# Kernel tuning notes

Measured on AMD Instinct MI355X. Metric: run time of the kernel, lower is better.

The kernel has to match this reference:

```python
import jax, jax.numpy as jnp
import numpy as np
from jax import lax

T, N, E = 12, 10000, 160000
C_IN, C_H, C_OUT = 32, 64, 32
EPS = 1e-5


def _glorot(key, shape):
    fan_in, fan_out = shape[-2] if len(shape) > 1 else shape[0], shape[-1]
    s = (6.0 / (fan_in + fan_out)) ** 0.5
    return jax.random.uniform(key, shape, jnp.float32, -s, s)


def setup_inputs() -> dict:
    key = jax.random.key(0)
    ks = jax.random.split(key, 16)
    inp = {
        "x": jax.random.normal(ks[0], (T, N, C_IN), jnp.float32),
        "edge_index": jax.random.randint(ks[1], (2, E), 0, N, jnp.int32),
        "edge_weight": jax.random.uniform(ks[2], (E,), jnp.float32),
        # layer 1 (input layer): in=C_IN -> C_H
        "conv_w1": _glorot(ks[3], (C_H, C_IN, 3)) * 0.1,
        "conv_b1": jnp.zeros((C_H,), jnp.float32),
        "gamma1": jnp.ones((C_H,), jnp.float32),
        "beta1": jnp.zeros((C_H,), jnp.float32),
        "gcn_w1": _glorot(ks[4], (C_H, C_H)),
        "gcn_b1": jnp.zeros((C_H,), jnp.float32),
        # layer 2 (hidden layer): C_H -> C_H
        "conv_w2": _glorot(ks[5], (C_H, C_H, 3)) * 0.1,
        "conv_b2": jnp.zeros((C_H,), jnp.float32),
        "gamma2": jnp.ones((C_H,), jnp.float32),
        "beta2": jnp.zeros((C_H,), jnp.float32),
        "gcn_w2": _glorot(ks[6], (C_H, C_H)),
        "gcn_b2": jnp.zeros((C_H,), jnp.float32),
        # output linear: C_H -> C_OUT
        "out_w": _glorot(ks[7], (C_H, C_OUT)),
        "out_b": jnp.zeros((C_OUT,), jnp.float32),
    }
    return inp


def _stgcn_layer(x, edge_index, edge_weight, cw, cb, gamma, beta, gw, gb):
    # x: [T, N, C_in]  ->  torch.stack(x).permute(1,2,0) = [N, C_in, T]
    xs = jnp.transpose(x, (1, 2, 0))
    h = lax.conv_general_dilated(xs, cw, (1,), [(1, 1)],
                                 dimension_numbers=("NCH", "OIH", "NCH"))
    h = h + cb[None, :, None]
    # InstanceNorm1d(affine) over the temporal dim
    mu = h.mean(-1, keepdims=True)
    var = ((h - mu) ** 2).mean(-1, keepdims=True)
    h = (h - mu) * lax.rsqrt(var + EPS) * gamma[None, :, None] + beta[None, :, None]
    h = jax.nn.relu(h)
    h = jnp.transpose(h, (2, 0, 1))  # [T, N, C_out]
    # GCNConv per timestep (vectorized over T)
    src, dst = edge_index[0], edge_index[1]
    n = h.shape[1]
    deg = jnp.zeros((n,), h.dtype).at[dst].add(edge_weight) + 1.0  # self-loop weight 1
    dis = lax.rsqrt(deg)
    norm = dis[src] * edge_weight * dis[dst]  # [E]
    xw = jnp.einsum("tnc,cd->tnd", h, gw)  # [T, N, C_out]
    msg = xw[:, src, :] * norm[None, :, None]  # [T, E, C_out]
    agg = jax.vmap(lambda m: jax.ops.segment_sum(m, dst, num_segments=n))(msg)
    agg = agg + (dis * dis)[None, :, None] * xw + gb  # self loop + bias
    return agg


def reference(x, edge_index, edge_weight,
              conv_w1, conv_b1, gamma1, beta1, gcn_w1, gcn_b1,
              conv_w2, conv_b2, gamma2, beta2, gcn_w2, gcn_b2,
              out_w, out_b):
    h = _stgcn_layer(x, edge_index, edge_weight,
                     conv_w1, conv_b1, gamma1, beta1, gcn_w1, gcn_b1)
    h = _stgcn_layer(h, edge_index, edge_weight,
                     conv_w2, conv_b2, gamma2, beta2, gcn_w2, gcn_b2)
    out = jnp.einsum("tnc,co->tno", h, out_w) + out_b  # per-t linear
    return out.mean(axis=0)  # [N, C_OUT]
```

## Files before the change

kernel.cpp:

```cpp
#include <hip/hip_runtime.h>
#include <hip/hip_bf16.h>
#include <stdint.h>

#define MAXDEG 64

typedef short s16x8 __attribute__((ext_vector_type(8)));
typedef short s16x4 __attribute__((ext_vector_type(4)));
typedef float f32x4 __attribute__((ext_vector_type(4)));

static __device__ __forceinline__ float us2f(unsigned short u) {
    union { float f; unsigned int i; } cv; cv.i = ((unsigned int)u) << 16; return cv.f;
}
static __device__ __forceinline__ unsigned short f2us(float f) {
    __hip_bfloat16 h = __float2bfloat16(f);
    return *(unsigned short*)&h;
}

#define WIMG_TOTAL 30720

__global__ void k_prep(const float* __restrict__ cw1, const float* __restrict__ gw1,
                       const float* __restrict__ cw2, const float* __restrict__ gw2,
                       unsigned short* __restrict__ wimg)
{
    int idx = blockIdx.x * 256 + threadIdx.x;
    if (idx >= WIMG_TOTAL) return;
    float v = 0.f;
    if (idx < 7680) {
        int kk = idx / 2560, r = idx - kk * 2560, cc = r / 40, ci = r - cc * 40;
        if (ci < 32) v = cw1[(cc * 32 + ci) * 3 + kk];
    } else if (idx < 12288) {
        int j = idx - 7680, d = j / 72, cc = j - d * 72;
        if (cc < 64) v = gw1[cc * 64 + d];
    } else if (idx < 26112) {
        int j = idx - 12288;
        int kk = j / 4608, r = j - kk * 4608, cc = r / 72, ci = r - cc * 72;
        if (ci < 64) v = cw2[(cc * 64 + ci) * 3 + kk];
    } else {
        int j = idx - 26112, d = j / 72, cc = j - d * 72;
        if (cc < 64) v = gw2[cc * 64 + d];
    }
    wimg[idx] = f2us(v);
}

#define BLO(u) __uint_as_float((unsigned)(u) << 16)
#define BHI(u) __uint_as_float((unsigned)(u) & 0xffff0000u)

#define ACC2(NRM, WA, WB)                                                              \
    a[0] = fmaf(NRM, BLO(WA.x), a[0]);   a[1] = fmaf(NRM, BHI(WA.x), a[1]);            \
    a[2] = fmaf(NRM, BLO(WA.y), a[2]);   a[3] = fmaf(NRM, BHI(WA.y), a[3]);            \
    a[4] = fmaf(NRM, BLO(WA.z), a[4]);   a[5] = fmaf(NRM, BHI(WA.z), a[5]);            \
    a[6] = fmaf(NRM, BLO(WA.w), a[6]);   a[7] = fmaf(NRM, BHI(WA.w), a[7]);            \
    a[8] = fmaf(NRM, us2f(WB.x), a[8]);  a[9] = fmaf(NRM, us2f(WB.y), a[9]);           \
    a[10] = fmaf(NRM, us2f(WB.z), a[10]); a[11] = fmaf(NRM, us2f(WB.w), a[11]);

template<int CIN>
__global__ __launch_bounds__(1024, 4) void k_layer_build(
    const float* __restrict__ x_in,
    const unsigned short* __restrict__ wimg,
    const float* __restrict__ gm, const float* __restrict__ bt,
    unsigned short* __restrict__ xw_out, int N, int NB,
    const int* __restrict__ ei, const float* __restrict__ ew,
    float* __restrict__ deg, unsigned* __restrict__ cnt,
    int2* __restrict__ ell, int E)
{
    if ((int)blockIdx.x >= NB) {
        int e = ((int)blockIdx.x - NB) * 1024 + (int)threadIdx.x;
        if (e < E) {
            int s = ei[e], d = ei[E + e];
            float w = ew[e];
            atomicAdd(&deg[d], w);
            unsigned slot = atomicAdd(&cnt[d], 1u);
            if (slot < MAXDEG) ell[(size_t)d * MAXDEG + slot] = make_int2(s, __float_as_int(w));
        }
        return;
    }

    constexpr int KT   = CIN / 32;
    constexpr int WSTR = (CIN == 64) ? 72 : 40;
    __shared__ __align__(16) short WT[3 * 64 * WSTR];
    __shared__ __align__(16) short gwT[64 * 72];
    __shared__ __align__(16) short xh[16][14 * 72];

    const int tid = threadIdx.x;
    const int nn = tid >> 6;
    const int c = tid & 63;
    const int m = c & 15;
    const int q = c >> 4;
    const int mrow = (m < 12) ? m : 11;
    int n = blockIdx.x * 16 + nn;
    if (n >= N) n = N - 1;

    {
        const uint4* wt1  = (const uint4*)(wimg);
        const uint4* gwt1 = (const uint4*)(wimg + 7680);
        if (tid < 960) ((uint4*)WT)[tid]  = wt1[tid];
        if (tid < 576) ((uint4*)gwT)[tid] = gwt1[tid];
    }
    #pragma unroll
    for (int it = 0; it < (12 * CIN) / 128; ++it) {
        int i2 = it * 128 + c * 2;
        int t = i2 / CIN, ci = i2 - t * CIN;
        float2 xv = *(const float2*)&x_in[((size_t)t * N + n) * CIN + ci];
        xh[nn][(t + 1) * 72 + ci]     = (short)f2us(xv.x);
        xh[nn][(t + 1) * 72 + ci + 1] = (short)f2us(xv.y);
    }
    if (c < CIN) { xh[nn][c] = 0; xh[nn][13 * 72 + c] = 0; }
    __syncthreads();

    f32x4 acc[4];
    #pragma unroll
    for (int nt = 0; nt < 4; ++nt) acc[nt] = (f32x4){0.f, 0.f, 0.f, 0.f};
    #pragma unroll
    for (int kk = 0; kk < 3; ++kk) {
        #pragma unroll
        for (int kt = 0; kt < KT; ++kt) {
            s16x8 aA = *(const s16x8*)&xh[nn][(mrow + kk) * 72 + kt * 32 + q * 8];
            #pragma unroll
            for (int nt = 0; nt < 4; ++nt) {
                s16x8 bB = *(const s16x8*)&WT[kk * (64 * WSTR) + (nt * 16 + m) * WSTR + kt * 32 + q * 8];
                acc[nt] = __builtin_amdgcn_mfma_f32_16x16x32_bf16(aA, bB, acc[nt], 0, 0, 0);
            }
        }
    }

    #pragma unroll
    for (int nt = 0; nt < 4; ++nt) {
        float s  = acc[nt][0] + acc[nt][1] + acc[nt][2] + acc[nt][3];
        float s2 = acc[nt][0] * acc[nt][0] + acc[nt][1] * acc[nt][1]
                 + acc[nt][2] * acc[nt][2] + acc[nt][3] * acc[nt][3];
        if (q == 3) { s = 0.f; s2 = 0.f; }
        s  += __shfl_xor(s, 16);  s  += __shfl_xor(s, 32);
        s2 += __shfl_xor(s2, 16); s2 += __shfl_xor(s2, 32);
        const float mu  = s * (1.f / 12.f);
        const float var = s2 * (1.f / 12.f) - mu * mu;
        const float scn = rsqrtf(var + 1e-5f) * gm[nt * 16 + m];
        const float sbn = bt[nt * 16 + m];
        if (q < 3) {
            #pragma unroll
            for (int reg = 0; reg < 4; ++reg) {
                float hv = fmaf(acc[nt][reg] - mu, scn, sbn);
                hv = hv > 0.f ? hv : 0.f;
                xh[nn][(q * 4 + reg) * 72 + nt * 16 + m] = (short)f2us(hv);
            }
        }
    }

    s16x8 a2[2];
    #pragma unroll
    for (int kt2 = 0; kt2 < 2; ++kt2)
        a2[kt2] = *(const s16x8*)&xh[nn][mrow * 72 + kt2 * 32 + q * 8];
    f32x4 acc2[4];
    #pragma unroll
    for (int nt = 0; nt < 4; ++nt) acc2[nt] = (f32x4){0.f, 0.f, 0.f, 0.f};
    #pragma unroll
    for (int nt = 0; nt < 4; ++nt) {
        #pragma unroll
        for (int kt2 = 0; kt2 < 2; ++kt2) {
            s16x8 b2 = *(const s16x8*)&gwT[(nt * 16 + m) * 72 + kt2 * 32 + q * 8];
            acc2[nt] = __builtin_amdgcn_mfma_f32_16x16x32_bf16(a2[kt2], b2, acc2[nt], 0, 0, 0);
        }
    }

    unsigned short* dst = xw_out + (size_t)n * 768;
    if (q < 3) {
        #pragma unroll
        for (int nt = 0; nt < 4; ++nt)
            #pragma unroll
            for (int reg = 0; reg < 4; ++reg)
                dst[(q * 4 + reg) * 64 + nt * 16 + m] = f2us(acc2[nt][reg]);
    }
}

__global__ __launch_bounds__(512, 4) void k_gather_a(
    const unsigned short* __restrict__ xw_in,
    const int2* __restrict__ ell, const unsigned* __restrict__ cnt,
    const float* __restrict__ deg, const float* __restrict__ gb,
    const unsigned short* __restrict__ wimg,
    const float* __restrict__ gm, const float* __restrict__ bt,
    unsigned short* __restrict__ rowmean, int N)
{
    constexpr int WSTR = 72;
    __shared__ __align__(16) short WT[3 * 64 * WSTR];
    __shared__ __align__(16) short gwT[64 * 72];
    __shared__ __align__(16) short xh[8][14 * 72];

    const int tid = threadIdx.x;
    const int nn = tid >> 6;
    const int L = tid & 63;
    const int m = L & 15;
    const int q = L >> 4;
    const int mrow = (m < 12) ? m : 11;
    int n = blockIdx.x * 8 + nn;
    if (n >= N) n = N - 1;

    const int2* row = ell + (size_t)n * MAXDEG;
    int2 pl = row[L];
    unsigned dg = cnt[n]; if (dg > MAXDEG) dg = MAXDEG;
    const float dn = rsqrtf(deg[n] + 1.0f);
    const float d2 = dn * dn;
    const unsigned short* sp = xw_in + (size_t)n * 768;
    uint4   sA = *(const uint4*)(sp + 8 * L);
    ushort4 sB = *(const ushort4*)(sp + 512 + 4 * L);

    {
        const uint4* wt2  = (const uint4*)(wimg + 12288);
        const uint4* gwt2 = (const uint4*)(wimg + 26112);
        for (int g = tid; g < 1728; g += 512) ((uint4*)WT)[g]  = wt2[g];
        for (int g = tid; g < 576;  g += 512) ((uint4*)gwT)[g] = gwt2[g];
    }
    xh[nn][L] = 0; xh[nn][13 * 72 + L] = 0;
    __syncthreads();

    float a[12];
    {
        const int cb1 = 8 * (L & 7);
        const int cb2 = (4 * L) & 63;
        a[0] = fmaf(d2, BLO(sA.x), gb[cb1 + 0]); a[1] = fmaf(d2, BHI(sA.x), gb[cb1 + 1]);
        a[2] = fmaf(d2, BLO(sA.y), gb[cb1 + 2]); a[3] = fmaf(d2, BHI(sA.y), gb[cb1 + 3]);
        a[4] = fmaf(d2, BLO(sA.z), gb[cb1 + 4]); a[5] = fmaf(d2, BHI(sA.z), gb[cb1 + 5]);
        a[6] = fmaf(d2, BLO(sA.w), gb[cb1 + 6]); a[7] = fmaf(d2, BHI(sA.w), gb[cb1 + 7]);
        a[8] = fmaf(d2, us2f(sB.x), gb[cb2 + 0]); a[9]  = fmaf(d2, us2f(sB.y), gb[cb2 + 1]);
        a[10] = fmaf(d2, us2f(sB.z), gb[cb2 + 2]); a[11] = fmaf(d2, us2f(sB.w), gb[cb2 + 3]);
    }

    unsigned e = 0;
    for (; e + 8 <= dg; e += 8) {
        uint4 A[8]; ushort4 Bv[8]; float NR[8];
        #pragma unroll
        for (int i = 0; i < 8; ++i) {
            unsigned sxr = (unsigned)__builtin_amdgcn_readlane(pl.x, (int)(e + i));
            float w = __int_as_float(__builtin_amdgcn_readlane(pl.y, (int)(e + i)));
            unsigned sx = (sxr < (unsigned)N) ? sxr : 0u;
            float nr = rsqrtf(deg[sx] + 1.0f) * w * dn;
            NR[i] = (sxr < (unsigned)N) ? nr : 0.f;
            const unsigned short* qp = xw_in + (size_t)sx * 768;
            A[i]  = *(const uint4*)(qp + 8 * L);
            Bv[i] = *(const ushort4*)(qp + 512 + 4 * L);
        }
        #pragma unroll
        for (int i = 0; i < 8; ++i) { ACC2(NR[i], A[i], Bv[i]) }
    }
    if (e + 4 <= dg) {
        uint4 A[4]; ushort4 Bv[4]; float NR[4];
        #pragma unroll
        for (int i = 0; i < 4; ++i) {
            unsigned sxr = (unsigned)__builtin_amdgcn_readlane(pl.x, (int)(e + i));
            float w = __int_as_float(__builtin_amdgcn_readlane(pl.y, (int)(e + i)));
            unsigned sx = (sxr < (unsigned)N) ? sxr : 0u;
            float nr = rsqrtf(deg[sx] + 1.0f) * w * dn;
            NR[i] = (sxr < (unsigned)N) ? nr : 0.f;
            const unsigned short* qp = xw_in + (size_t)sx * 768;
            A[i]  = *(const uint4*)(qp + 8 * L);
            Bv[i] = *(const ushort4*)(qp + 512 + 4 * L);
        }
        #pragma unroll
        for (int i = 0; i < 4; ++i) { ACC2(NR[i], A[i], Bv[i]) }
        e += 4;
    }
    for (; e < dg; ++e) {
        unsigned sxr = (unsigned)__builtin_amdgcn_readlane(pl.x, (int)e);
        float w = __int_as_float(__builtin_amdgcn_readlane(pl.y, (int)e));
        unsigned sx = (sxr < (unsigned)N) ? sxr : 0u;
        float nr = rsqrtf(deg[sx] + 1.0f) * w * dn;
        if (sxr >= (unsigned)N) nr = 0.f;
        const unsigned short* qp = xw_in + (size_t)sx * 768;
        uint4 A = *(const uint4*)(qp + 8 * L);
        ushort4 Bv = *(const ushort4*)(qp + 512 + 4 * L);
        ACC2(nr, A, Bv)
    }

    {
        s16x8 p1 = { (short)f2us(a[0]), (short)f2us(a[1]), (short)f2us(a[2]), (short)f2us(a[3]),
                     (short)f2us(a[4]), (short)f2us(a[5]), (short)f2us(a[6]), (short)f2us(a[7]) };
        *(s16x8*)&xh[nn][((L >> 3) + 1) * 72 + 8 * (L & 7)] = p1;
        s16x4 p2 = { (short)f2us(a[8]), (short)f2us(a[9]), (short)f2us(a[10]), (short)f2us(a[11]) };
        *(s16x4*)&xh[nn][((L >> 4) + 9) * 72 + ((4 * L) & 63)] = p2;
    }

    f32x4 acc[4];
    #pragma unroll
    for (int nt = 0; nt < 4; ++nt) acc[nt] = (f32x4){0.f, 0.f, 0.f, 0.f};
    #pragma unroll
    for (int kk = 0; kk < 3; ++kk) {
        #pragma unroll
        for (int kt = 0; kt < 2; ++kt) {
            s16x8 aA = *(const s16x8*)&xh[nn][(mrow + kk) * 72 + kt * 32 + q * 8];
            #pragma unroll
            for (int nt = 0; nt < 4; ++nt) {
                s16x8 bB = *(const s16x8*)&WT[kk * (64 * WSTR) + (nt * 16 + m) * WSTR + kt * 32 + q * 8];
                acc[nt] = __builtin_amdgcn_mfma_f32_16x16x32_bf16(aA, bB, acc[nt], 0, 0, 0);
            }
        }
    }

    #pragma unroll
    for (int nt = 0; nt < 4; ++nt) {
        float s  = acc[nt][0] + acc[nt][1] + acc[nt][2] + acc[nt][3];
        float s2 = acc[nt][0] * acc[nt][0] + acc[nt][1] * acc[nt][1]
                 + acc[nt][2] * acc[nt][2] + acc[nt][3] * acc[nt][3];
        if (q == 3) { s = 0.f; s2 = 0.f; }
        s  += __shfl_xor(s, 16);  s  += __shfl_xor(s, 32);
        s2 += __shfl_xor(s2, 16); s2 += __shfl_xor(s2, 32);
        const float mu  = s * (1.f / 12.f);
        const float var = s2 * (1.f / 12.f) - mu * mu;
        const float scn = rsqrtf(var + 1e-5f) * gm[nt * 16 + m];
        const float sbn = bt[nt * 16 + m];
        if (q < 3) {
            #pragma unroll
            for (int reg = 0; reg < 4; ++reg) {
                float hv = fmaf(acc[nt][reg] - mu, scn, sbn);
                hv = hv > 0.f ? hv : 0.f;
                xh[nn][(q * 4 + reg) * 72 + nt * 16 + m] = (short)f2us(hv);
            }
        }
    }

    s16x8 a2[2];
    #pragma unroll
    for (int kt2 = 0; kt2 < 2; ++kt2)
        a2[kt2] = *(const s16x8*)&xh[nn][mrow * 72 + kt2 * 32 + q * 8];
    f32x4 acc2[4];
    #pragma unroll
    for (int nt = 0; nt < 4; ++nt) acc2[nt] = (f32x4){0.f, 0.f, 0.f, 0.f};
    #pragma unroll
    for (int nt = 0; nt < 4; ++nt) {
        #pragma unroll
        for (int kt2 = 0; kt2 < 2; ++kt2) {
            s16x8 b2 = *(const s16x8*)&gwT[(nt * 16 + m) * 72 + kt2 * 32 + q * 8];
            acc2[nt] = __builtin_amdgcn_mfma_f32_16x16x32_bf16(a2[kt2], b2, acc2[nt], 0, 0, 0);
        }
    }

    #pragma unroll
    for (int nt = 0; nt < 4; ++nt) {
        float pm = (q < 3) ? (acc2[nt][0] + acc2[nt][1] + acc2[nt][2] + acc2[nt][3]) : 0.f;
        pm += __shfl_xor(pm, 16); pm += __shfl_xor(pm, 32);
        if (q == 0)
            rowmean[(size_t)n * 64 + nt * 16 + m] = f2us(pm * (1.f / 12.f));
    }
}

#define FIN_E(EIDX)                                                                    \
    {                                                                                  \
        unsigned sxr = (unsigned)__builtin_amdgcn_readlane(pl.x, (int)(EIDX));         \
        float w = __int_as_float(__builtin_amdgcn_readlane(pl.y, (int)(EIDX)));        \
        unsigned sx = (sxr < (unsigned)N) ? sxr : 0u;                                  \
        float nr = rsqrtf(deg[sx] + 1.0f) * w * dn;                                    \
        if (sxr >= (unsigned)N) nr = 0.f;                                              \
        a = fmaf(nr, us2f(rowmean[(size_t)sx * 64 + L]), a);                           \
    }

__global__ __launch_bounds__(256) void k_final(
    const unsigned short* __restrict__ rowmean, const int2* __restrict__ ell,
    const unsigned* __restrict__ cnt, const float* __restrict__ deg,
    const float* __restrict__ gb,
    const float* __restrict__ ow, const float* __restrict__ ob,
    float* __restrict__ dout, int N)
{
    __shared__ __align__(16) float hbuf[4][64];
    const int tid = threadIdx.x;
    const int nn = tid >> 6, L = tid & 63;
    int n = blockIdx.x * 4 + nn;
    if (n >= N) n = N - 1;
    const float dn = rsqrtf(deg[n] + 1.0f);
    const float d2 = dn * dn;

    const int2* row = ell + (size_t)n * MAXDEG;
    int2 pl = row[L];
    unsigned dg = cnt[n]; if (dg > MAXDEG) dg = MAXDEG;

    float a = fmaf(d2, us2f(rowmean[(size_t)n * 64 + L]), gb[L]);

    unsigned e = 0;
    for (; e + 7 < dg; e += 8) {
        FIN_E(e)     FIN_E(e + 1) FIN_E(e + 2) FIN_E(e + 3)
        FIN_E(e + 4) FIN_E(e + 5) FIN_E(e + 6) FIN_E(e + 7)
    }
    for (; e < dg; ++e) { FIN_E(e) }

    hbuf[nn][L] = a;
    __syncthreads();
    if (L < 32) {
        float oa = ob[L];
        #pragma unroll
        for (int cc = 0; cc < 64; ++cc)
            oa = fmaf(hbuf[nn][cc], ow[cc * 32 + L], oa);
        dout[(size_t)n * 32 + L] = oa;
    }
}

extern "C" void kernel_launch(void* const* d_in, const int* in_sizes, int n_in,
                              void* d_out, int out_size, void* d_ws, size_t ws_size,
                              hipStream_t stream)
{
    const float* x   = (const float*)d_in[0];
    const int*   ei  = (const int*)d_in[1];
    const float* ew  = (const float*)d_in[2];
    const float* cw1 = (const float*)d_in[3];
    const float* gm1 = (const float*)d_in[5];
    const float* bt1 = (const float*)d_in[6];
    const float* gw1 = (const float*)d_in[7];
    const float* gb1 = (const float*)d_in[8];
    const float* cw2 = (const float*)d_in[9];
    const float* gm2 = (const float*)d_in[11];
    const float* bt2 = (const float*)d_in[12];
    const float* gw2 = (const float*)d_in[13];
    const float* gb2 = (const float*)d_in[14];
    const float* ow  = (const float*)d_in[15];
    const float* ob  = (const float*)d_in[16];

    const int N = in_sizes[0] / (12 * 32);
    const int E = in_sizes[2];

    char* p0 = (char*)d_ws;
    char* p = p0;
    float* deg = (float*)p;          p += (size_t)N * 4;
    unsigned* cnt = (unsigned*)p;    p += (size_t)N * 4;
    p = (char*)(((uintptr_t)p + 255) & ~(uintptr_t)255);
    int2* ell = (int2*)p;            p += (size_t)N * MAXDEG * 8;
    p = (char*)(((uintptr_t)p + 255) & ~(uintptr_t)255);
    unsigned short* wimg = (unsigned short*)p; p += (size_t)WIMG_TOTAL * 2;
    p = (char*)(((uintptr_t)p + 255) & ~(uintptr_t)255);
    unsigned short* bufXW1 = (unsigned short*)p; p += (size_t)N * 768 * 2;
    unsigned short* rowmean = (unsigned short*)p; p += (size_t)N * 64 * 2;

    const size_t need = (size_t)(p - p0);
    if (ws_size < need) {
        hipMemsetAsync(d_out, 0, (size_t)out_size * 4, stream);
        return;
    }

    hipMemsetAsync(deg, 0, (size_t)N * 8, stream);

    const int nb16 = (N + 15) / 16;
    const int ebb  = (E + 1023) / 1024;
    const int nb8  = (N + 7) / 8;
    const int nb4  = (N + 3) / 4;
    k_prep<<<(WIMG_TOTAL + 255) / 256, 256, 0, stream>>>(cw1, gw1, cw2, gw2, wimg);

    k_layer_build<32><<<nb16 + ebb, 1024, 0, stream>>>(x, wimg, gm1, bt1, bufXW1, N, nb16,
                                                       ei, ew, deg, cnt, ell, E);
    k_gather_a<<<nb8, 512, 0, stream>>>(bufXW1, ell, cnt, deg, gb1,
                                        wimg, gm2, bt2, rowmean, N);
    k_final<<<nb4, 256, 0, stream>>>(rowmean, ell, cnt, deg, gb2, ow, ob, (float*)d_out, N);
}
```

Before: 169.6 us.

## Fold output linear into layer-2 GCN weight and aggregate 32-wide rowmeans

Precomputes gw2·out_w (64x32) and a constant bias gb2·out_w+ob in the prep kernel, so layer 2 produces 32-channel projected rowmeans instead of 64. The final gather then reads half as much data per neighbor and drops the per-node 64x32 matvec and its shared-memory sync. The deg/cnt zeroing memset is also folded into the prep kernel to remove one launch. The fused weight is rounded to bf16, which changes rounding slightly.

```diff
diff --git a/kernel.cpp b/kernel.cpp
--- a/kernel.cpp
+++ b/kernel.cpp
@@ -16,30 +16,47 @@
     return *(unsigned short*)&h;
 }
 
-#define WIMG_TOTAL 30720
+#define WIMG_TOTAL 28416
 
 __global__ void k_prep(const float* __restrict__ cw1, const float* __restrict__ gw1,
                        const float* __restrict__ cw2, const float* __restrict__ gw2,
-                       unsigned short* __restrict__ wimg)
+                       const float* __restrict__ gb2, const float* __restrict__ ow,
+                       const float* __restrict__ ob,
+                       unsigned short* __restrict__ wimg, float* __restrict__ c0f,
+                       unsigned* __restrict__ zbase, int zwords)
 {
     int idx = blockIdx.x * 256 + threadIdx.x;
-    if (idx >= WIMG_TOTAL) return;
-    float v = 0.f;
-    if (idx < 7680) {
-        int kk = idx / 2560, r = idx - kk * 2560, cc = r / 40, ci = r - cc * 40;
-        if (ci < 32) v = cw1[(cc * 32 + ci) * 3 + kk];
-    } else if (idx < 12288) {
-        int j = idx - 7680, d = j / 72, cc = j - d * 72;
-        if (cc < 64) v = gw1[cc * 64 + d];
-    } else if (idx < 26112) {
-        int j = idx - 12288;
-        int kk = j / 4608, r = j - kk * 4608, cc = r / 72, ci = r - cc * 72;
-        if (ci < 64) v = cw2[(cc * 64 + ci) * 3 + kk];
-    } else {
-        int j = idx - 26112, d = j / 72, cc = j - d * 72;
-        if (cc < 64) v = gw2[cc * 64 + d];
-    }
-    wimg[idx] = f2us(v);
+    if (idx < WIMG_TOTAL) {
+        float v = 0.f;
+        if (idx < 7680) {
+            int kk = idx / 2560, r = idx - kk * 2560, cc = r / 40, ci = r - cc * 40;
+            if (ci < 32) v = cw1[(cc * 32 + ci) * 3 + kk];
+        } else if (idx < 12288) {
+            int j = idx - 7680, d = j / 72, cc = j - d * 72;
+            if (cc < 64) v = gw1[cc * 64 + d];
+        } else if (idx < 26112) {
+            int j = idx - 12288;
+            int kk = j / 4608, r = j - kk * 4608, cc = r / 72, ci = r - cc * 72;
+            if (ci < 64) v = cw2[(cc * 64 + ci) * 3 + kk];
+        } else {
+            int j = idx - 26112, o = j / 72, cc = j - o * 72;
+            if (cc < 64) {
+                float s = 0.f;
+                #pragma unroll 8
+                for (int d = 0; d < 64; ++d) s = fmaf(gw2[cc * 64 + d], ow[d * 32 + o], s);
+                v = s;
+            }
+        }
+        wimg[idx] = f2us(v);
+    } else if (idx < WIMG_TOTAL + 32) {
+        int o = idx - WIMG_TOTAL;
+        float s = ob[o];
+        #pragma unroll 8
+        for (int c = 0; c < 64; ++c) s = fmaf(gb2[c], ow[c * 32 + o], s);
+        c0f[o] = s;
+    } else if (idx - (WIMG_TOTAL + 32) < zwords) {
+        zbase[idx - (WIMG_TOTAL + 32)] = 0u;
+    }
 }
 
 #define BLO(u) __uint_as_float((unsigned)(u) << 16)
@@ -177,11 +194,11 @@
     const float* __restrict__ deg, const float* __restrict__ gb,
     const unsigned short* __restrict__ wimg,
     const float* __restrict__ gm, const float* __restrict__ bt,
-    unsigned short* __restrict__ rowmean, int N)
+    unsigned short* __restrict__ rm32, int N)
 {
     constexpr int WSTR = 72;
     __shared__ __align__(16) short WT[3 * 64 * WSTR];
-    __shared__ __align__(16) short gwT[64 * 72];
+    __shared__ __align__(16) short gwT[32 * 72];
     __shared__ __align__(16) short xh[8][14 * 72];
 
     const int tid = threadIdx.x;
@@ -204,9 +221,9 @@
 
     {
         const uint4* wt2  = (const uint4*)(wimg + 12288);
-        const uint4* gwt2 = (const uint4*)(wimg + 26112);
+        const uint4* gwp  = (const uint4*)(wimg + 26112);
         for (int g = tid; g < 1728; g += 512) ((uint4*)WT)[g]  = wt2[g];
-        for (int g = tid; g < 576;  g += 512) ((uint4*)gwT)[g] = gwt2[g];
+        if (tid < 288) ((uint4*)gwT)[tid] = gwp[tid];
     }
     xh[nn][L] = 0; xh[nn][13 * 72 + L] = 0;
     __syncthreads();
@@ -319,11 +336,11 @@
     #pragma unroll
     for (int kt2 = 0; kt2 < 2; ++kt2)
         a2[kt2] = *(const s16x8*)&xh[nn][mrow * 72 + kt2 * 32 + q * 8];
-    f32x4 acc2[4];
-    #pragma unroll
-    for (int nt = 0; nt < 4; ++nt) acc2[nt] = (f32x4){0.f, 0.f, 0.f, 0.f};
-    #pragma unroll
-    for (int nt = 0; nt < 4; ++nt) {
+    f32x4 acc2[2];
+    acc2[0] = (f32x4){0.f, 0.f, 0.f, 0.f};
+    acc2[1] = (f32x4){0.f, 0.f, 0.f, 0.f};
+    #pragma unroll
+    for (int nt = 0; nt < 2; ++nt) {
         #pragma unroll
         for (int kt2 = 0; kt2 < 2; ++kt2) {
             s16x8 b2 = *(const s16x8*)&gwT[(nt * 16 + m) * 72 + kt2 * 32 + q * 8];
@@ -332,11 +349,11 @@
     }
 
     #pragma unroll
-    for (int nt = 0; nt < 4; ++nt) {
+    for (int nt = 0; nt < 2; ++nt) {
         float pm = (q < 3) ? (acc2[nt][0] + acc2[nt][1] + acc2[nt][2] + acc2[nt][3]) : 0.f;
         pm += __shfl_xor(pm, 16); pm += __shfl_xor(pm, 32);
         if (q == 0)
-            rowmean[(size_t)n * 64 + nt * 16 + m] = f2us(pm * (1.f / 12.f));
+            rm32[(size_t)n * 32 + nt * 16 + m] = f2us(pm * (1.f / 12.f));
     }
 }
 
@@ -347,19 +364,18 @@
         unsigned sx = (sxr < (unsigned)N) ? sxr : 0u;                                  \
         float nr = rsqrtf(deg[sx] + 1.0f) * w * dn;                                    \
         if (sxr >= (unsigned)N) nr = 0.f;                                              \
-        a = fmaf(nr, us2f(rowmean[(size_t)sx * 64 + L]), a);                           \
+        a = fmaf(nr, us2f(rm32[(size_t)sx * 32 + o]), a);                              \
     }
 
 __global__ __launch_bounds__(256) void k_final(
-    const unsigned short* __restrict__ rowmean, const int2* __restrict__ ell,
+    const unsigned short* __restrict__ rm32, const int2* __restrict__ ell,
     const unsigned* __restrict__ cnt, const float* __restrict__ deg,
-    const float* __restrict__ gb,
-    const float* __restrict__ ow, const float* __restrict__ ob,
+    const float* __restrict__ c0f,
     float* __restrict__ dout, int N)
 {
-    __shared__ __align__(16) float hbuf[4][64];
     const int tid = threadIdx.x;
     const int nn = tid >> 6, L = tid & 63;
+    const int o = L & 31;
     int n = blockIdx.x * 4 + nn;
     if (n >= N) n = N - 1;
     const float dn = rsqrtf(deg[n] + 1.0f);
@@ -369,7 +385,7 @@
     int2 pl = row[L];
     unsigned dg = cnt[n]; if (dg > MAXDEG) dg = MAXDEG;
 
-    float a = fmaf(d2, us2f(rowmean[(size_t)n * 64 + L]), gb[L]);
+    float a = fmaf(d2, us2f(rm32[(size_t)n * 32 + o]), c0f[o]);
 
     unsigned e = 0;
     for (; e + 7 < dg; e += 8) {
@@ -378,15 +394,7 @@
     }
     for (; e < dg; ++e) { FIN_E(e) }
 
-    hbuf[nn][L] = a;
-    __syncthreads();
-    if (L < 32) {
-        float oa = ob[L];
-        #pragma unroll
-        for (int cc = 0; cc < 64; ++cc)
-            oa = fmaf(hbuf[nn][cc], ow[cc * 32 + L], oa);
-        dout[(size_t)n * 32 + L] = oa;
-    }
+    if (L < 32) dout[(size_t)n * 32 + o] = a;
 }
 
 extern "C" void kernel_launch(void* const* d_in, const int* in_sizes, int n_in,
@@ -421,8 +429,10 @@
     p = (char*)(((uintptr_t)p + 255) & ~(uintptr_t)255);
     unsigned short* wimg = (unsigned short*)p; p += (size_t)WIMG_TOTAL * 2;
     p = (char*)(((uintptr_t)p + 255) & ~(uintptr_t)255);
+    float* c0f = (float*)p;          p += 32 * 4;
+    p = (char*)(((uintptr_t)p + 255) & ~(uintptr_t)255);
     unsigned short* bufXW1 = (unsigned short*)p; p += (size_t)N * 768 * 2;
-    unsigned short* rowmean = (unsigned short*)p; p += (size_t)N * 64 * 2;
+    unsigned short* rm32 = (unsigned short*)p;   p += (size_t)N * 32 * 2;
 
     const size_t need = (size_t)(p - p0);
     if (ws_size < need) {
@@ -430,17 +440,18 @@
         return;
     }
 
-    hipMemsetAsync(deg, 0, (size_t)N * 8, stream);
-
+    const int zwords = 2 * N;
+    const int prep_tot = WIMG_TOTAL + 32 + zwords;
     const int nb16 = (N + 15) / 16;
     const int ebb  = (E + 1023) / 1024;
     const int nb8  = (N + 7) / 8;
     const int nb4  = (N + 3) / 4;
-    k_prep<<<(WIMG_TOTAL + 255) / 256, 256, 0, stream>>>(cw1, gw1, cw2, gw2, wimg);
-
+
+    k_prep<<<(prep_tot + 255) / 256, 256, 0, stream>>>(cw1, gw1, cw2, gw2, gb2, ow, ob,
+                                                       wimg, c0f, (unsigned*)deg, zwords);
     k_layer_build<32><<<nb16 + ebb, 1024, 0, stream>>>(x, wimg, gm1, bt1, bufXW1, N, nb16,
                                                        ei, ew, deg, cnt, ell, E);
     k_gather_a<<<nb8, 512, 0, stream>>>(bufXW1, ell, cnt, deg, gb1,
-                                        wimg, gm2, bt2, rowmean, N);
-    k_final<<<nb4, 256, 0, stream>>>(rowmean, ell, cnt, deg, gb2, ow, ob, (float*)d_out, N);
-}
+                                        wimg, gm2, bt2, rm32, N);
+    k_final<<<nb4, 256, 0, stream>>>(rm32, ell, cnt, deg, c0f, (float*)d_out, N);
+}
```

Measured after the change: 167.8 us. Within noise of the previous version (-1.1%).
